# Kernel optimization log

Measured on AMD Instinct MI355X. Metric: run time of the kernel, lower is better.

Reference implementation:

```python
import jax, jax.numpy as jnp
import numpy as np

N = 20000      # nodes
E = 100000     # edges
B = 128        # graphs in batch
F_IN = 14      # node feature dim
DIM = 64       # hidden dim
E_FEAT = 4     # edge feature dim
MLP_H = 128    # edge MLP hidden


def setup_inputs() -> dict:
    key = jax.random.key(0)
    ks = jax.random.split(key, 26)

    def rn(k, shape, fan_in):
        return jax.random.normal(k, shape, jnp.float32) / np.sqrt(fan_in)

    d = {}
    d['x'] = jax.random.normal(ks[0], (N, F_IN), jnp.float32)
    d['edge_attr'] = jax.random.uniform(ks[1], (E, E_FEAT), jnp.float32)
    d['edge_index'] = jax.random.randint(ks[2], (2, E), 0, N)
    d['batch'] = jnp.sort(jax.random.randint(ks[3], (N,), 0, B))
    # lin0
    d['lin0_w'] = rn(ks[4], (F_IN, DIM), F_IN)
    d['lin0_b'] = jnp.zeros((DIM,), jnp.float32)
    # edge MLP: Linear(4,128) -> ReLU -> Linear(128, dim*dim)
    d['mlp_w1'] = rn(ks[5], (E_FEAT, MLP_H), E_FEAT)
    d['mlp_b1'] = jnp.zeros((MLP_H,), jnp.float32)
    d['mlp_w2'] = rn(ks[6], (MLP_H, DIM * DIM), MLP_H) * 0.1
    d['mlp_b2'] = jnp.zeros((DIM * DIM,), jnp.float32)
    # NNConv root weight + bias
    d['conv_root'] = rn(ks[7], (DIM, DIM), DIM)
    d['conv_bias'] = jnp.zeros((DIM,), jnp.float32)
    # GRU (input dim DIM, hidden DIM), torch gate order r,z,n
    d['gru_wi'] = rn(ks[8], (DIM, 3 * DIM), DIM)
    d['gru_wh'] = rn(ks[9], (DIM, 3 * DIM), DIM)
    d['gru_bi'] = jnp.zeros((3 * DIM,), jnp.float32)
    d['gru_bh'] = jnp.zeros((3 * DIM,), jnp.float32)
    # Set2Set LSTM (input 2*DIM, hidden DIM), torch gate order i,f,g,o
    d['lstm_wi'] = rn(ks[10], (2 * DIM, 4 * DIM), 2 * DIM)
    d['lstm_wh'] = rn(ks[11], (DIM, 4 * DIM), DIM)
    d['lstm_bi'] = jnp.zeros((4 * DIM,), jnp.float32)
    d['lstm_bh'] = jnp.zeros((4 * DIM,), jnp.float32)
    # output head
    d['lin1_w'] = rn(ks[12], (2 * DIM, DIM), 2 * DIM)
    d['lin1_b'] = jnp.zeros((DIM,), jnp.float32)
    d['lin2_w'] = rn(ks[13], (DIM, 1), DIM)
    d['lin2_b'] = jnp.zeros((1,), jnp.float32)
    return d


def _forward(x, edge_attr, edge_index, batch,
             lin0_w, lin0_b, mlp_w1, mlp_b1, mlp_w2, mlp_b2,
             conv_root, conv_bias,
             gru_wi, gru_wh, gru_bi, gru_bh,
             lstm_wi, lstm_wh, lstm_bi, lstm_bh,
             lin1_w, lin1_b, lin2_w, lin2_b):
    src, dst = edge_index[0], edge_index[1]

    out = jax.nn.relu(x @ lin0_w + lin0_b)            # [N, DIM]
    h = out                                            # GRU hidden

    # per-edge weight matrices from edge MLP (shared across the 3 steps)
    ew = jax.nn.relu(edge_attr @ mlp_w1 + mlp_b1) @ mlp_w2 + mlp_b2
    ew = ew.reshape(E, DIM, DIM)                       # [E, DIM, DIM]
    # incoming-edge counts for scatter-mean
    cnt = jax.ops.segment_sum(jnp.ones((E,), jnp.float32), dst, num_segments=N)
    cnt = jnp.maximum(cnt, 1.0)[:, None]

    for _ in range(3):
        msg = jnp.einsum('ei,eio->eo', out[src], ew)   # gather + per-edge matmul
        agg = jax.ops.segment_sum(msg, dst, num_segments=N) / cnt
        m = jax.nn.relu(agg + out @ conv_root + conv_bias)
        # GRU cell (torch gate order: r, z, n)
        gi = m @ gru_wi + gru_bi
        gh = h @ gru_wh + gru_bh
        r = jax.nn.sigmoid(gi[:, :DIM] + gh[:, :DIM])
        z = jax.nn.sigmoid(gi[:, DIM:2 * DIM] + gh[:, DIM:2 * DIM])
        n = jnp.tanh(gi[:, 2 * DIM:] + r * gh[:, 2 * DIM:])
        h = (1.0 - z) * n + z * h
        out = h

    # Set2Set pooling, 3 processing steps
    q_star = jnp.zeros((B, 2 * DIM), jnp.float32)
    hl = jnp.zeros((B, DIM), jnp.float32)
    cl = jnp.zeros((B, DIM), jnp.float32)
    for _ in range(3):
        gates = q_star @ lstm_wi + hl @ lstm_wh + lstm_bi + lstm_bh  # [B, 4*DIM]
        i = jax.nn.sigmoid(gates[:, :DIM])
        f = jax.nn.sigmoid(gates[:, DIM:2 * DIM])
        g = jnp.tanh(gates[:, 2 * DIM:3 * DIM])
        o = jax.nn.sigmoid(gates[:, 3 * DIM:])
        cl = f * cl + i * g
        hl = o * jnp.tanh(cl)
        q = hl                                         # [B, DIM]
        e = jnp.sum(out * q[batch], axis=-1)           # [N]
        emax = jax.ops.segment_max(e, batch, num_segments=B)
        emax = jnp.where(jnp.isfinite(emax), emax, 0.0)
        a = jnp.exp(e - emax[batch])
        asum = jax.ops.segment_sum(a, batch, num_segments=B)
        a = a / jnp.maximum(asum, 1e-16)[batch]
        r_vec = jax.ops.segment_sum(a[:, None] * out, batch, num_segments=B)
        q_star = jnp.concatenate([q, r_vec], axis=-1)  # [B, 2*DIM]

    y = jax.nn.relu(q_star @ lin1_w + lin1_b) @ lin2_w + lin2_b
    return y.reshape(-1)                               # [B]


def reference(x, edge_attr, edge_index, batch,
              lin0_w, lin0_b, mlp_w1, mlp_b1, mlp_w2, mlp_b2,
              conv_root, conv_bias,
              gru_wi, gru_wh, gru_bi, gru_bh,
              lstm_wi, lstm_wh, lstm_bi, lstm_bh,
              lin1_w, lin1_b, lin2_w, lin2_b):
    return _forward(x, edge_attr, edge_index, batch,
                    lin0_w, lin0_b, mlp_w1, mlp_b1, mlp_w2, mlp_b2,
                    conv_root, conv_bias,
                    gru_wi, gru_wh, gru_bi, gru_bh,
                    lstm_wi, lstm_wh, lstm_bi, lstm_bh,
                    lin1_w, lin1_b, lin2_w, lin2_b)
```

## Files before the change

kernel.cpp:

```cpp
#include <hip/hip_runtime.h>
#include <math.h>

#define N_ 20000
#define E_ 100000
#define B_ 128
#define F_IN_ 14
#define DIM_ 64
#define E_FEAT_ 4
#define MLP_H_ 128
#define EWC_ 4096
#define PC_ 8192
#define PC2_ 8256

typedef __attribute__((ext_vector_type(4))) float f32x4;
typedef __attribute__((ext_vector_type(8))) _Float16 halfx8;

__global__ void lin0_kernel(const float* __restrict__ x, const float* __restrict__ w,
                            const float* __restrict__ b, float* __restrict__ out) {
    int idx = blockIdx.x * blockDim.x + threadIdx.x;
    if (idx >= N_ * DIM_) return;
    int n = idx >> 6, d = idx & 63;
    float acc = b[d];
#pragma unroll
    for (int f = 0; f < F_IN_; ++f) acc = fmaf(x[n * F_IN_ + f], w[f * DIM_ + d], acc);
    out[idx] = acc > 0.f ? acc : 0.f;
}

__global__ void mlp1_kernel(const float* __restrict__ ea, const float* __restrict__ w1,
                            const float* __restrict__ b1, const int* __restrict__ epos,
                            _Float16* __restrict__ h1s) {
    int idx = blockIdx.x * blockDim.x + threadIdx.x;
    if (idx >= E_ * MLP_H_) return;
    int e = idx >> 7, k = idx & 127;
    float acc = b1[k];
#pragma unroll
    for (int f = 0; f < E_FEAT_; ++f) acc = fmaf(ea[e * E_FEAT_ + f], w1[f * MLP_H_ + k], acc);
    h1s[(size_t)epos[e] * 128 + k] = (_Float16)(acc > 0.f ? acc : 0.f);
}

__global__ void deg_kernel(const int* __restrict__ src, const int* __restrict__ dst,
                           float* __restrict__ cnt, int* __restrict__ cnt_src) {
    int e = blockIdx.x * blockDim.x + threadIdx.x;
    if (e >= E_) return;
    atomicAdd(&cnt[dst[e]], 1.0f);
    atomicAdd(&cnt_src[src[e]], 1);
}

__global__ void batch_off_kernel(const int* __restrict__ batch, int* __restrict__ off_b) {
    int b = threadIdx.x;
    if (b > B_) return;
    int lo = 0, hi = N_;
    while (lo < hi) {
        int mid = (lo + hi) >> 1;
        if (batch[mid] < b) lo = mid + 1; else hi = mid;
    }
    off_b[b] = lo;
}

__global__ void scan_src(const int* __restrict__ cnt_src, int* __restrict__ src_off) {
    __shared__ int part[256];
    __shared__ int off[257];
    int t = threadIdx.x;
    const int per = (N_ + 255) / 256;
    int base = t * per;
    int s = 0;
    for (int i = 0; i < per; ++i) { int b = base + i; if (b < N_) s += cnt_src[b]; }
    part[t] = s;
    __syncthreads();
    if (t == 0) {
        int a = 0;
        for (int i = 0; i < 256; ++i) { off[i] = a; a += part[i]; }
        off[256] = a;
    }
    __syncthreads();
    int run = off[t];
    for (int i = 0; i < per; ++i) {
        int b = base + i;
        if (b < N_) { src_off[b] = run; run += cnt_src[b]; }
    }
    if (t == 0) src_off[N_] = off[256];
}

__global__ void scatter_src(const int* __restrict__ src, const int* __restrict__ dst,
                            int* __restrict__ cur, const int* __restrict__ src_off,
                            int* __restrict__ epos, int* __restrict__ dsts) {
    int e = blockIdx.x * blockDim.x + threadIdx.x;
    if (e >= E_) return;
    int s = src[e];
    int p = src_off[s] + atomicAdd(&cur[s], 1);
    epos[e] = p;
    dsts[p] = dst[e];
}

__global__ void prep_b(const float* __restrict__ w2, const float* __restrict__ b2,
                       _Float16* __restrict__ Bf) {
    int idx = blockIdx.x * blockDim.x + threadIdx.x;
    if (idx >= PC2_ * 64) return;
    int c16 = idx >> 10;
    int r   = idx & 1023;
    int ks  = r >> 9;
    int q   = (r >> 7) & 3;
    int lr  = (r >> 3) & 15;
    int j   = r & 7;
    int c = c16 * 16 + lr;
    int i = ks * 32 + q * 8 + j;
    float v;
    if (c < PC_) {
        int o = c >> 7, k = c & 127;
        v = w2[(size_t)k * EWC_ + i * 64 + o];
    } else {
        int o = c - PC_;
        v = b2[i * 64 + o];
    }
    Bf[idx] = (_Float16)v;
}

__global__ __launch_bounds__(512, 4) void fused_msg(
        const float* __restrict__ out, const _Float16* __restrict__ Bf,
        const _Float16* __restrict__ h1s,
        const int* __restrict__ dsts, const int* __restrict__ src_off,
        float* __restrict__ agg) {
    __shared__ _Float16 Plds[16 * 2048];
    const int tid = threadIdx.x;
    const int lane = tid & 63;
    const int w = __builtin_amdgcn_readfirstlane(tid >> 6);
    const int lrow = lane & 15, quad = lane >> 4;
    const int nb0 = blockIdx.x * 16;

    halfx8 aG[2];
    {
        const float* orow = out + (size_t)(nb0 + lrow) * 64 + quad * 8;
#pragma unroll
        for (int ks = 0; ks < 2; ++ks) {
            float4 v0 = *(const float4*)(orow + ks * 32);
            float4 v1 = *(const float4*)(orow + ks * 32 + 4);
            aG[ks][0] = (_Float16)v0.x; aG[ks][1] = (_Float16)v0.y;
            aG[ks][2] = (_Float16)v0.z; aG[ks][3] = (_Float16)v0.w;
            aG[ks][4] = (_Float16)v1.x; aG[ks][5] = (_Float16)v1.y;
            aG[ks][6] = (_Float16)v1.z; aG[ks][7] = (_Float16)v1.w;
        }
    }

    f32x4 qf[4];
#pragma unroll
    for (int f = 0; f < 4; ++f) {
        const _Float16* bc = &Bf[(size_t)(512 + f) * 1024 + quad * 128 + lrow * 8];
        halfx8 bq0 = *(const halfx8*)bc;
        halfx8 bq1 = *(const halfx8*)(bc + 512);
        f32x4 z = (f32x4){0.f, 0.f, 0.f, 0.f};
        z = __builtin_amdgcn_mfma_f32_16x16x32_f16(aG[0], bq0, z, 0, 0, 0);
        z = __builtin_amdgcn_mfma_f32_16x16x32_f16(aG[1], bq1, z, 0, 0, 0);
        qf[f] = z;
    }

    const int n0g = nb0 + 2 * w;
    const int beg0 = src_off[n0g];
    const int end0 = src_off[n0g + 1];
    const int end1 = src_off[n0g + 2];

#pragma unroll
    for (int p = 0; p < 4; ++p) {
        if (p) __syncthreads();

#pragma unroll 8
        for (int nf = 0; nf < 16; ++nf) {
            int cl = w * 256 + nf * 16 + lrow;
            size_t tb = (size_t)(p * 128 + w * 16 + nf) * 1024 + quad * 128 + lrow * 8;
            halfx8 b0 = *(const halfx8*)&Bf[tb];
            halfx8 b1 = *(const halfx8*)&Bf[tb + 512];
            f32x4 acc = (f32x4){0.f, 0.f, 0.f, 0.f};
            acc = __builtin_amdgcn_mfma_f32_16x16x32_f16(aG[0], b0, acc, 0, 0, 0);
            acc = __builtin_amdgcn_mfma_f32_16x16x32_f16(aG[1], b1, acc, 0, 0, 0);
            int o = cl >> 7, k = cl & 127;
            int kz = k ^ (quad << 5) ^ ((o & 7) << 3);
            int base = o * 2048 + kz;
#pragma unroll
            for (int rr = 0; rr < 4; ++rr)
                Plds[base + (quad * 4 + rr) * 128] = (_Float16)acc[rr];
        }
        __syncthreads();

        int o0 = p * 16;
#pragma unroll
        for (int nn = 0; nn < 2; ++nn) {
            int nl = 2 * w + nn;
            int beg = nn ? end0 : beg0;
            int endv = nn ? end1 : end0;
            if (beg == endv) continue;
            int srcl = ((nl >> 2) << 4) | lrow;
            int rsel = nl & 3;
            float qel = rsel == 0 ? qf[p][0] : rsel == 1 ? qf[p][1]
                      : rsel == 2 ? qf[p][2] : qf[p][3];
            float qv = __shfl(qel, srcl, 64);
            halfx8 bf[4];
#pragma unroll
            for (int ks = 0; ks < 4; ++ks) {
                int kk = (ks * 32 + quad * 8) ^ ((nl >> 2) << 5) ^ ((lrow & 7) << 3);
                bf[ks] = *(const halfx8*)&Plds[lrow * 2048 + nl * 128 + kk];
            }
            for (int g = beg; g < endv; g += 16) {
                int gcnt = endv - g; if (gcnt > 16) gcnt = 16;
                int ei = lrow < gcnt ? lrow : gcnt - 1;
                int gi = g + ei;
                int dv = dsts[gi];
                halfx8 af[4];
#pragma unroll
                for (int ks = 0; ks < 4; ++ks)
                    af[ks] = *(const halfx8*)&h1s[(size_t)gi * 128 + ks * 32 + quad * 8];
                f32x4 acc = (f32x4){0.f, 0.f, 0.f, 0.f};
#pragma unroll
                for (int ks = 0; ks < 4; ++ks)
                    acc = __builtin_amdgcn_mfma_f32_16x16x32_f16(
                        af[ks], bf[ks], acc, 0, 0, 0);
#pragma unroll
                for (int rr = 0; rr < 4; ++rr) {
                    int j = quad * 4 + rr;
                    int d = __shfl(dv, j, 64);
                    if (j < gcnt) {
                        atomicAdd(&agg[(size_t)d * 64 + o0 + lrow], acc[rr] + qv);
                    }
                }
            }
        }
    }
}

__global__ __launch_bounds__(256) void gru_kernel(float* __restrict__ out,
                                                  float* __restrict__ agg,
                                                  const float* __restrict__ cnt,
                                                  const float* __restrict__ root,
                                                  const float* __restrict__ cbias,
                                                  const float* __restrict__ wi,
                                                  const float* __restrict__ wh,
                                                  const float* __restrict__ bi,
                                                  const float* __restrict__ bh) {
    __shared__ float root_s[64 * 64];
    __shared__ float h_s[32 * 64];
    __shared__ float m_s[32 * 64];
    int tid = threadIdx.x;
    int lane = tid & 63;
    int wv = __builtin_amdgcn_readfirstlane(tid >> 6);
    int nb = blockIdx.x * 32;
#pragma unroll
    for (int it = 0; it < 4; ++it) {
        int i = it * 1024 + tid * 4;
        *(float4*)&root_s[i] = *(const float4*)&root[i];
    }
#pragma unroll
    for (int it = 0; it < 2; ++it) {
        int i = it * 1024 + tid * 4;
        *(float4*)&h_s[i] = *(const float4*)&out[(size_t)nb * 64 + i];
    }
    __syncthreads();

    int nbase = nb + wv * 8;
    float a[8];
#pragma unroll
    for (int j = 0; j < 8; ++j) {
        int n = nbase + j;
        float c = cnt[n]; c = c > 1.f ? c : 1.f;
        a[j] = agg[(size_t)n * 64 + lane] / c + cbias[lane];
        agg[(size_t)n * 64 + lane] = 0.f;
    }
    for (int i = 0; i < 64; ++i) {
        float rv = root_s[i * 64 + lane];
#pragma unroll
        for (int j = 0; j < 8; ++j)
            a[j] = fmaf(h_s[(wv * 8 + j) * 64 + i], rv, a[j]);
    }
#pragma unroll
    for (int j = 0; j < 8; ++j) {
        float m = a[j] > 0.f ? a[j] : 0.f;
        m_s[(wv * 8 + j) * 64 + lane] = m;
    }
    __syncthreads();

    float gir[8], giz[8], gin[8], ghr[8], ghz[8], ghn[8];
    float bi0 = bi[lane], bi1 = bi[64 + lane], bi2 = bi[128 + lane];
    float bh0 = bh[lane], bh1 = bh[64 + lane], bh2 = bh[128 + lane];
#pragma unroll
    for (int j = 0; j < 8; ++j) {
        gir[j] = bi0; giz[j] = bi1; gin[j] = bi2;
        ghr[j] = bh0; ghz[j] = bh1; ghn[j] = bh2;
    }
    for (int i = 0; i < 64; ++i) {
        float w0 = wi[i * 192 + lane];
        float w1 = wi[i * 192 + 64 + lane];
        float w2v = wi[i * 192 + 128 + lane];
        float u0 = wh[i * 192 + lane];
        float u1 = wh[i * 192 + 64 + lane];
        float u2 = wh[i * 192 + 128 + lane];
#pragma unroll
        for (int j = 0; j < 8; ++j) {
            float mi = m_s[(wv * 8 + j) * 64 + i];
            float hi = h_s[(wv * 8 + j) * 64 + i];
            gir[j] = fmaf(mi, w0, gir[j]);
            giz[j] = fmaf(mi, w1, giz[j]);
            gin[j] = fmaf(mi, w2v, gin[j]);
            ghr[j] = fmaf(hi, u0, ghr[j]);
            ghz[j] = fmaf(hi, u1, ghz[j]);
            ghn[j] = fmaf(hi, u2, ghn[j]);
        }
    }
#pragma unroll
    for (int j = 0; j < 8; ++j) {
        int n = nbase + j;
        float rg = 1.f / (1.f + expf(-(gir[j] + ghr[j])));
        float zg = 1.f / (1.f + expf(-(giz[j] + ghz[j])));
        float ng = tanhf(gin[j] + rg * ghn[j]);
        float h = h_s[(wv * 8 + j) * 64 + lane];
        out[(size_t)n * 64 + lane] = (1.f - zg) * ng + zg * h;
    }
}

__global__ __launch_bounds__(256) void lstm_attn_kernel(
        const float* __restrict__ out, const int* __restrict__ off_b,
        float* __restrict__ hl, float* __restrict__ cl,
        float* __restrict__ q_star, float* __restrict__ e_ws,
        const float* __restrict__ wi, const float* __restrict__ wh,
        const float* __restrict__ bi, const float* __restrict__ bh,
        const float* __restrict__ hw1, const float* __restrict__ hb1,
        const float* __restrict__ hw2, const float* __restrict__ hb2,
        float* __restrict__ y, int do_head) {
    int b = blockIdx.x;
    int t = threadIdx.x;
    __shared__ float qs[128], hs[64], g[256];
    __shared__ float q[64];
    __shared__ float red[256], racc[256], sasum[4];

    if (t < 128) qs[t] = q_star[b * 128 + t];
    if (t < 64) hs[t] = hl[b * 64 + t];
    __syncthreads();
    {
        float acc = bi[t] + bh[t];
#pragma unroll 8
        for (int i = 0; i < 128; ++i) acc = fmaf(qs[i], wi[i * 256 + t], acc);
#pragma unroll 8
        for (int i = 0; i < 64; ++i) acc = fmaf(hs[i], wh[i * 256 + t], acc);
        g[t] = acc;
    }
    __syncthreads();
    if (t < 64) {
        float ig = 1.f / (1.f + expf(-g[t]));
        float fg = 1.f / (1.f + expf(-g[64 + t]));
        float gg = tanhf(g[128 + t]);
        float og = 1.f / (1.f + expf(-g[192 + t]));
        float c = fg * cl[b * 64 + t] + ig * gg;
        cl[b * 64 + t] = c;
        float h = og * tanhf(c);
        hl[b * 64 + t] = h;
        q[t] = h;
    }
    __syncthreads();

    int start = off_b[b], end = off_b[b + 1];
    float lmax = -1e30f;
    for (int n = start + t; n < end; n += 256) {
        float acc = 0.f;
#pragma unroll 16
        for (int d2 = 0; d2 < 64; ++d2) acc = fmaf(out[n * 64 + d2], q[d2], acc);
        e_ws[n] = acc;
        lmax = fmaxf(lmax, acc);
    }
    red[t] = lmax;
    __syncthreads();
    for (int s2 = 128; s2 > 0; s2 >>= 1) {
        if (t < s2) red[t] = fmaxf(red[t], red[t + s2]);
        __syncthreads();
    }
    float emax = red[0];
    int w = t >> 6, d = t & 63;
    float rl = 0.f, lasum = 0.f;
    for (int n = start + w; n < end; n += 4) {
        float a = expf(e_ws[n] - emax);
        rl = fmaf(a, out[n * 64 + d], rl);
        if (d == 0) lasum += a;
    }
    racc[t] = rl;
    if (d == 0) sasum[w] = lasum;
    __syncthreads();
    if (t < 64) {
        float r = racc[t] + racc[64 + t] + racc[128 + t] + racc[192 + t];
        float as = sasum[0] + sasum[1] + sasum[2] + sasum[3];
        as = fmaxf(as, 1e-16f);
        float rv = r / as;
        q_star[b * 128 + t] = q[t];
        q_star[b * 128 + 64 + t] = rv;
        qs[t] = q[t];
        qs[64 + t] = rv;
    }
    __syncthreads();

    if (do_head && t < 64) {
        float acc = hb1[t];
#pragma unroll 8
        for (int i = 0; i < 128; ++i) acc = fmaf(qs[i], hw1[i * 64 + t], acc);
        acc = acc > 0.f ? acc : 0.f;
        float p = acc * hw2[t];
        for (int off = 32; off > 0; off >>= 1) p += __shfl_down(p, off, 64);
        if (t == 0) y[b] = p + hb2[0];
    }
}

extern "C" void kernel_launch(void* const* d_in, const int* in_sizes, int n_in,
                              void* d_out, int out_size, void* d_ws, size_t ws_size,
                              hipStream_t stream) {
    (void)in_sizes; (void)n_in; (void)out_size; (void)ws_size;
    const float* x        = (const float*)d_in[0];
    const float* ea       = (const float*)d_in[1];
    const int*   eidx     = (const int*)d_in[2];
    const int*   batch    = (const int*)d_in[3];
    const float* lin0_w   = (const float*)d_in[4];
    const float* lin0_b   = (const float*)d_in[5];
    const float* mlp_w1   = (const float*)d_in[6];
    const float* mlp_b1   = (const float*)d_in[7];
    const float* mlp_w2   = (const float*)d_in[8];
    const float* mlp_b2   = (const float*)d_in[9];
    const float* conv_root= (const float*)d_in[10];
    const float* conv_bias= (const float*)d_in[11];
    const float* gru_wi   = (const float*)d_in[12];
    const float* gru_wh   = (const float*)d_in[13];
    const float* gru_bi   = (const float*)d_in[14];
    const float* gru_bh   = (const float*)d_in[15];
    const float* lstm_wi  = (const float*)d_in[16];
    const float* lstm_wh  = (const float*)d_in[17];
    const float* lstm_bi  = (const float*)d_in[18];
    const float* lstm_bh  = (const float*)d_in[19];
    const float* lin1_w   = (const float*)d_in[20];
    const float* lin1_b   = (const float*)d_in[21];
    const float* lin2_w   = (const float*)d_in[22];
    const float* lin2_b   = (const float*)d_in[23];
    float* y = (float*)d_out;

    const int* src = eidx;
    const int* dst = eidx + E_;

    char* w = (char*)d_ws;
    auto carve = [&](size_t bytes) {
        char* p = w;
        w += (bytes + 255) & ~(size_t)255;
        return p;
    };
    float* out_buf = (float*)carve((size_t)N_ * DIM_ * 4);
    float* e_ws    = (float*)carve((size_t)N_ * 4);
    int*   off_b   = (int*)carve((size_t)(B_ + 1) * 4);
    _Float16* h1s  = (_Float16*)carve((size_t)E_ * MLP_H_ * 2);
    _Float16* Bf   = (_Float16*)carve((size_t)PC2_ * 64 * 2);
    int*   src_off = (int*)carve((size_t)(N_ + 1) * 4);
    int*   epos    = (int*)carve((size_t)E_ * 4);
    int*   dsts    = (int*)carve((size_t)E_ * 4);
    char*  zero0   = w;
    float* agg     = (float*)carve((size_t)N_ * DIM_ * 4);
    float* cnt     = (float*)carve((size_t)N_ * 4);
    int*   cnt_src = (int*)carve((size_t)N_ * 4);
    int*   cur     = (int*)carve((size_t)N_ * 4);
    float* q_star  = (float*)carve((size_t)B_ * 128 * 4);
    float* hl      = (float*)carve((size_t)B_ * 64 * 4);
    float* cl      = (float*)carve((size_t)B_ * 64 * 4);
    size_t zbytes  = (size_t)(w - zero0);

    hipMemsetAsync(zero0, 0, zbytes, stream);

    lin0_kernel<<<(N_ * DIM_ + 255) / 256, 256, 0, stream>>>(x, lin0_w, lin0_b, out_buf);
    deg_kernel<<<(E_ + 255) / 256, 256, 0, stream>>>(src, dst, cnt, cnt_src);
    batch_off_kernel<<<1, 256, 0, stream>>>(batch, off_b);
    scan_src<<<1, 256, 0, stream>>>(cnt_src, src_off);
    scatter_src<<<(E_ + 255) / 256, 256, 0, stream>>>(src, dst, cur, src_off, epos, dsts);
    mlp1_kernel<<<(E_ * MLP_H_ + 255) / 256, 256, 0, stream>>>(ea, mlp_w1, mlp_b1, epos, h1s);
    prep_b<<<(PC2_ * 64 + 255) / 256, 256, 0, stream>>>(mlp_w2, mlp_b2, Bf);

    for (int step = 0; step < 3; ++step) {
        fused_msg<<<N_ / 16, 512, 0, stream>>>(out_buf, Bf, h1s, dsts,
                                               src_off, agg);
        gru_kernel<<<N_ / 32, 256, 0, stream>>>(out_buf, agg, cnt, conv_root, conv_bias,
                                                gru_wi, gru_wh, gru_bi, gru_bh);
    }

    for (int s = 0; s < 3; ++s) {
        lstm_attn_kernel<<<B_, 256, 0, stream>>>(out_buf, off_b, hl, cl, q_star, e_ws,
                                                 lstm_wi, lstm_wh, lstm_bi, lstm_bh,
                                                 lin1_w, lin1_b, lin2_w, lin2_b,
                                                 y, s == 2 ? 1 : 0);
    }
}
```

Measured before the change: 603.9 us.

## Process 32 source nodes per block to reuse weight tiles across two node groups

```diff
diff --git a/kernel.cpp b/kernel.cpp
--- a/kernel.cpp
+++ b/kernel.cpp
@@ -120,83 +120,105 @@
         const _Float16* __restrict__ h1s,
         const int* __restrict__ dsts, const int* __restrict__ src_off,
         float* __restrict__ agg) {
-    __shared__ _Float16 Plds[16 * 2048];
+    __shared__ _Float16 Plds[8 * 4096];
     const int tid = threadIdx.x;
     const int lane = tid & 63;
     const int w = __builtin_amdgcn_readfirstlane(tid >> 6);
     const int lrow = lane & 15, quad = lane >> 4;
-    const int nb0 = blockIdx.x * 16;
-
-    halfx8 aG[2];
+    const int lr7 = lrow & 7;
+    const int nb0 = blockIdx.x * 32;
+
+    halfx8 aA[2], aB[2];
     {
-        const float* orow = out + (size_t)(nb0 + lrow) * 64 + quad * 8;
+        const float* orowA = out + (size_t)(nb0 + lrow) * 64 + quad * 8;
+        const float* orowB = out + (size_t)(nb0 + 16 + lrow) * 64 + quad * 8;
 #pragma unroll
         for (int ks = 0; ks < 2; ++ks) {
-            float4 v0 = *(const float4*)(orow + ks * 32);
-            float4 v1 = *(const float4*)(orow + ks * 32 + 4);
-            aG[ks][0] = (_Float16)v0.x; aG[ks][1] = (_Float16)v0.y;
-            aG[ks][2] = (_Float16)v0.z; aG[ks][3] = (_Float16)v0.w;
-            aG[ks][4] = (_Float16)v1.x; aG[ks][5] = (_Float16)v1.y;
-            aG[ks][6] = (_Float16)v1.z; aG[ks][7] = (_Float16)v1.w;
+            float4 v0 = *(const float4*)(orowA + ks * 32);
+            float4 v1 = *(const float4*)(orowA + ks * 32 + 4);
+            aA[ks][0] = (_Float16)v0.x; aA[ks][1] = (_Float16)v0.y;
+            aA[ks][2] = (_Float16)v0.z; aA[ks][3] = (_Float16)v0.w;
+            aA[ks][4] = (_Float16)v1.x; aA[ks][5] = (_Float16)v1.y;
+            aA[ks][6] = (_Float16)v1.z; aA[ks][7] = (_Float16)v1.w;
+            float4 u0 = *(const float4*)(orowB + ks * 32);
+            float4 u1 = *(const float4*)(orowB + ks * 32 + 4);
+            aB[ks][0] = (_Float16)u0.x; aB[ks][1] = (_Float16)u0.y;
+            aB[ks][2] = (_Float16)u0.z; aB[ks][3] = (_Float16)u0.w;
+            aB[ks][4] = (_Float16)u1.x; aB[ks][5] = (_Float16)u1.y;
+            aB[ks][6] = (_Float16)u1.z; aB[ks][7] = (_Float16)u1.w;
         }
     }
 
-    f32x4 qf[4];
+    f32x4 qfA[4], qfB[4];
 #pragma unroll
     for (int f = 0; f < 4; ++f) {
         const _Float16* bc = &Bf[(size_t)(512 + f) * 1024 + quad * 128 + lrow * 8];
         halfx8 bq0 = *(const halfx8*)bc;
         halfx8 bq1 = *(const halfx8*)(bc + 512);
         f32x4 z = (f32x4){0.f, 0.f, 0.f, 0.f};
-        z = __builtin_amdgcn_mfma_f32_16x16x32_f16(aG[0], bq0, z, 0, 0, 0);
-        z = __builtin_amdgcn_mfma_f32_16x16x32_f16(aG[1], bq1, z, 0, 0, 0);
-        qf[f] = z;
-    }
-
-    const int n0g = nb0 + 2 * w;
-    const int beg0 = src_off[n0g];
-    const int end0 = src_off[n0g + 1];
-    const int end1 = src_off[n0g + 2];
-
-#pragma unroll
-    for (int p = 0; p < 4; ++p) {
+        z = __builtin_amdgcn_mfma_f32_16x16x32_f16(aA[0], bq0, z, 0, 0, 0);
+        z = __builtin_amdgcn_mfma_f32_16x16x32_f16(aA[1], bq1, z, 0, 0, 0);
+        qfA[f] = z;
+        f32x4 z2 = (f32x4){0.f, 0.f, 0.f, 0.f};
+        z2 = __builtin_amdgcn_mfma_f32_16x16x32_f16(aB[0], bq0, z2, 0, 0, 0);
+        z2 = __builtin_amdgcn_mfma_f32_16x16x32_f16(aB[1], bq1, z2, 0, 0, 0);
+        qfB[f] = z2;
+    }
+
+    const int nA = nb0 + 2 * w;
+    const int nB = nb0 + 16 + 2 * w;
+    const int begA0 = src_off[nA], endA0 = src_off[nA + 1], endA1 = src_off[nA + 2];
+    const int begB0 = src_off[nB], endB0 = src_off[nB + 1], endB1 = src_off[nB + 2];
+
+#pragma unroll
+    for (int p = 0; p < 8; ++p) {
         if (p) __syncthreads();
 
-#pragma unroll 8
-        for (int nf = 0; nf < 16; ++nf) {
-            int cl = w * 256 + nf * 16 + lrow;
-            size_t tb = (size_t)(p * 128 + w * 16 + nf) * 1024 + quad * 128 + lrow * 8;
+#pragma unroll
+        for (int it = 0; it < 8; ++it) {
+            int f64 = w * 8 + it;
+            size_t tb = (size_t)(p * 64 + f64) * 1024 + quad * 128 + lrow * 8;
             halfx8 b0 = *(const halfx8*)&Bf[tb];
             halfx8 b1 = *(const halfx8*)&Bf[tb + 512];
-            f32x4 acc = (f32x4){0.f, 0.f, 0.f, 0.f};
-            acc = __builtin_amdgcn_mfma_f32_16x16x32_f16(aG[0], b0, acc, 0, 0, 0);
-            acc = __builtin_amdgcn_mfma_f32_16x16x32_f16(aG[1], b1, acc, 0, 0, 0);
+            f32x4 accA = (f32x4){0.f, 0.f, 0.f, 0.f};
+            f32x4 accB = (f32x4){0.f, 0.f, 0.f, 0.f};
+            accA = __builtin_amdgcn_mfma_f32_16x16x32_f16(aA[0], b0, accA, 0, 0, 0);
+            accA = __builtin_amdgcn_mfma_f32_16x16x32_f16(aA[1], b1, accA, 0, 0, 0);
+            accB = __builtin_amdgcn_mfma_f32_16x16x32_f16(aB[0], b0, accB, 0, 0, 0);
+            accB = __builtin_amdgcn_mfma_f32_16x16x32_f16(aB[1], b1, accB, 0, 0, 0);
+            int cl = f64 * 16 + lrow;
             int o = cl >> 7, k = cl & 127;
-            int kz = k ^ (quad << 5) ^ ((o & 7) << 3);
-            int base = o * 2048 + kz;
-#pragma unroll
-            for (int rr = 0; rr < 4; ++rr)
-                Plds[base + (quad * 4 + rr) * 128] = (_Float16)acc[rr];
+            int kz = k ^ (quad << 5) ^ (o << 3);
+            int base = o * 4096 + kz;
+#pragma unroll
+            for (int rr = 0; rr < 4; ++rr) {
+                Plds[base + (quad * 4 + rr) * 128] = (_Float16)accA[rr];
+                Plds[base + (16 + quad * 4 + rr) * 128] = (_Float16)accB[rr];
+            }
         }
         __syncthreads();
 
-        int o0 = p * 16;
-#pragma unroll
-        for (int nn = 0; nn < 2; ++nn) {
-            int nl = 2 * w + nn;
-            int beg = nn ? end0 : beg0;
-            int endv = nn ? end1 : end0;
+        int o0 = p * 8;
+#pragma unroll
+        for (int nn = 0; nn < 4; ++nn) {
+            int nl15 = 2 * w + (nn & 1);
+            int nl = ((nn >> 1) << 4) | nl15;
+            int beg  = (nn == 0) ? begA0 : (nn == 1) ? endA0
+                     : (nn == 2) ? begB0 : endB0;
+            int endv = (nn == 0) ? endA0 : (nn == 1) ? endA1
+                     : (nn == 2) ? endB0 : endB1;
             if (beg == endv) continue;
-            int srcl = ((nl >> 2) << 4) | lrow;
-            int rsel = nl & 3;
-            float qel = rsel == 0 ? qf[p][0] : rsel == 1 ? qf[p][1]
-                      : rsel == 2 ? qf[p][2] : qf[p][3];
+            f32x4 qq = (nn >> 1) ? qfB[p >> 1] : qfA[p >> 1];
+            int rsel = nl15 & 3;
+            float qel = rsel == 0 ? qq[0] : rsel == 1 ? qq[1]
+                      : rsel == 2 ? qq[2] : qq[3];
+            int srcl = ((nl15 >> 2) << 4) | (((p & 1) << 3) | lr7);
             float qv = __shfl(qel, srcl, 64);
             halfx8 bf[4];
 #pragma unroll
             for (int ks = 0; ks < 4; ++ks) {
-                int kk = (ks * 32 + quad * 8) ^ ((nl >> 2) << 5) ^ ((lrow & 7) << 3);
-                bf[ks] = *(const halfx8*)&Plds[lrow * 2048 + nl * 128 + kk];
+                int kk = (ks * 32 + quad * 8) ^ (((nl >> 2) & 3) << 5) ^ (lr7 << 3);
+                bf[ks] = *(const halfx8*)&Plds[lr7 * 4096 + nl * 128 + kk];
             }
             for (int g = beg; g < endv; g += 16) {
                 int gcnt = endv - g; if (gcnt > 16) gcnt = 16;
@@ -216,8 +238,8 @@
                 for (int rr = 0; rr < 4; ++rr) {
                     int j = quad * 4 + rr;
                     int d = __shfl(dv, j, 64);
-                    if (j < gcnt) {
-                        atomicAdd(&agg[(size_t)d * 64 + o0 + lrow], acc[rr] + qv);
+                    if (j < gcnt && lrow < 8) {
+                        atomicAdd(&agg[(size_t)d * 64 + o0 + lr7], acc[rr] + qv);
                     }
                 }
             }
@@ -470,7 +492,7 @@
     prep_b<<<(PC2_ * 64 + 255) / 256, 256, 0, stream>>>(mlp_w2, mlp_b2, Bf);
 
     for (int step = 0; step < 3; ++step) {
-        fused_msg<<<N_ / 16, 512, 0, stream>>>(out_buf, Bf, h1s, dsts,
+        fused_msg<<<N_ / 32, 512, 0, stream>>>(out_buf, Bf, h1s, dsts,
                                                src_off, agg);
         gru_kernel<<<N_ / 32, 256, 0, stream>>>(out_buf, agg, cnt, conv_root, conv_bias,
                                                 gru_wi, gru_wh, gru_bi, gru_bh);
```

New measurement: 696.4 us. +15.3%, slower.

## Fuse setup kernels and merge three Set2Set LSTM steps into one launch

Applied to the files above, without the earlier changes.

```diff
diff --git a/kernel.cpp b/kernel.cpp
--- a/kernel.cpp
+++ b/kernel.cpp
@@ -26,35 +26,23 @@
     out[idx] = acc > 0.f ? acc : 0.f;
 }
 
-__global__ void mlp1_kernel(const float* __restrict__ ea, const float* __restrict__ w1,
-                            const float* __restrict__ b1, const int* __restrict__ epos,
-                            _Float16* __restrict__ h1s) {
-    int idx = blockIdx.x * blockDim.x + threadIdx.x;
-    if (idx >= E_ * MLP_H_) return;
-    int e = idx >> 7, k = idx & 127;
-    float acc = b1[k];
-#pragma unroll
-    for (int f = 0; f < E_FEAT_; ++f) acc = fmaf(ea[e * E_FEAT_ + f], w1[f * MLP_H_ + k], acc);
-    h1s[(size_t)epos[e] * 128 + k] = (_Float16)(acc > 0.f ? acc : 0.f);
-}
-
-__global__ void deg_kernel(const int* __restrict__ src, const int* __restrict__ dst,
-                           float* __restrict__ cnt, int* __restrict__ cnt_src) {
+__global__ void deg_boff_kernel(const int* __restrict__ src, const int* __restrict__ dst,
+                                float* __restrict__ cnt, int* __restrict__ cnt_src,
+                                const int* __restrict__ batch, int* __restrict__ off_b) {
     int e = blockIdx.x * blockDim.x + threadIdx.x;
-    if (e >= E_) return;
-    atomicAdd(&cnt[dst[e]], 1.0f);
-    atomicAdd(&cnt_src[src[e]], 1);
-}
-
-__global__ void batch_off_kernel(const int* __restrict__ batch, int* __restrict__ off_b) {
-    int b = threadIdx.x;
-    if (b > B_) return;
-    int lo = 0, hi = N_;
-    while (lo < hi) {
-        int mid = (lo + hi) >> 1;
-        if (batch[mid] < b) lo = mid + 1; else hi = mid;
-    }
-    off_b[b] = lo;
+    if (e < E_) {
+        atomicAdd(&cnt[dst[e]], 1.0f);
+        atomicAdd(&cnt_src[src[e]], 1);
+    }
+    if (blockIdx.x == 0 && threadIdx.x <= B_) {
+        int b = threadIdx.x;
+        int lo = 0, hi = N_;
+        while (lo < hi) {
+            int mid = (lo + hi) >> 1;
+            if (batch[mid] < b) lo = mid + 1; else hi = mid;
+        }
+        off_b[b] = lo;
+    }
 }
 
 __global__ void scan_src(const int* __restrict__ cnt_src, int* __restrict__ src_off) {
@@ -81,15 +69,41 @@
     if (t == 0) src_off[N_] = off[256];
 }
 
-__global__ void scatter_src(const int* __restrict__ src, const int* __restrict__ dst,
-                            int* __restrict__ cur, const int* __restrict__ src_off,
-                            int* __restrict__ epos, int* __restrict__ dsts) {
-    int e = blockIdx.x * blockDim.x + threadIdx.x;
+__global__ __launch_bounds__(256) void scatter_mlp1(
+        const int* __restrict__ src, const int* __restrict__ dst,
+        int* __restrict__ cur, const int* __restrict__ src_off,
+        const float* __restrict__ ea, const float* __restrict__ w1,
+        const float* __restrict__ b1, int* __restrict__ dsts,
+        _Float16* __restrict__ h1s) {
+    __shared__ float w1s[E_FEAT_ * MLP_H_];
+    __shared__ float b1s[MLP_H_];
+    int t = threadIdx.x;
+    if (t < MLP_H_) b1s[t] = b1[t];
+    for (int i = t; i < E_FEAT_ * MLP_H_; i += 256) w1s[i] = w1[i];
+    __syncthreads();
+    int e = blockIdx.x * 256 + t;
     if (e >= E_) return;
     int s = src[e];
     int p = src_off[s] + atomicAdd(&cur[s], 1);
-    epos[e] = p;
     dsts[p] = dst[e];
+    float a0 = ea[e * 4 + 0], a1 = ea[e * 4 + 1];
+    float a2 = ea[e * 4 + 2], a3 = ea[e * 4 + 3];
+    _Float16* hrow = h1s + (size_t)p * 128;
+#pragma unroll
+    for (int k8 = 0; k8 < 16; ++k8) {
+        halfx8 v;
+#pragma unroll
+        for (int j = 0; j < 8; ++j) {
+            int k = k8 * 8 + j;
+            float acc = b1s[k];
+            acc = fmaf(a0, w1s[k], acc);
+            acc = fmaf(a1, w1s[128 + k], acc);
+            acc = fmaf(a2, w1s[256 + k], acc);
+            acc = fmaf(a3, w1s[384 + k], acc);
+            v[j] = (_Float16)(acc > 0.f ? acc : 0.f);
+        }
+        *(halfx8*)&hrow[k8 * 8] = v;
+    }
 }
 
 __global__ void prep_b(const float* __restrict__ w2, const float* __restrict__ b2,
@@ -313,85 +327,85 @@
     }
 }
 
-__global__ __launch_bounds__(256) void lstm_attn_kernel(
+__global__ __launch_bounds__(256) void lstm_all_kernel(
         const float* __restrict__ out, const int* __restrict__ off_b,
-        float* __restrict__ hl, float* __restrict__ cl,
-        float* __restrict__ q_star, float* __restrict__ e_ws,
+        float* __restrict__ e_ws,
         const float* __restrict__ wi, const float* __restrict__ wh,
         const float* __restrict__ bi, const float* __restrict__ bh,
         const float* __restrict__ hw1, const float* __restrict__ hb1,
         const float* __restrict__ hw2, const float* __restrict__ hb2,
-        float* __restrict__ y, int do_head) {
+        float* __restrict__ y) {
     int b = blockIdx.x;
     int t = threadIdx.x;
-    __shared__ float qs[128], hs[64], g[256];
+    __shared__ float qs[128], hs[64], cs[64], g[256];
     __shared__ float q[64];
     __shared__ float red[256], racc[256], sasum[4];
 
-    if (t < 128) qs[t] = q_star[b * 128 + t];
-    if (t < 64) hs[t] = hl[b * 64 + t];
-    __syncthreads();
-    {
-        float acc = bi[t] + bh[t];
+    if (t < 128) qs[t] = 0.f;
+    if (t < 64) { hs[t] = 0.f; cs[t] = 0.f; }
+    __syncthreads();
+
+    int start = off_b[b], end = off_b[b + 1];
+
+    for (int s = 0; s < 3; ++s) {
+        {
+            float acc = bi[t] + bh[t];
 #pragma unroll 8
-        for (int i = 0; i < 128; ++i) acc = fmaf(qs[i], wi[i * 256 + t], acc);
+            for (int i = 0; i < 128; ++i) acc = fmaf(qs[i], wi[i * 256 + t], acc);
 #pragma unroll 8
-        for (int i = 0; i < 64; ++i) acc = fmaf(hs[i], wh[i * 256 + t], acc);
-        g[t] = acc;
-    }
-    __syncthreads();
+            for (int i = 0; i < 64; ++i) acc = fmaf(hs[i], wh[i * 256 + t], acc);
+            g[t] = acc;
+        }
+        __syncthreads();
+        if (t < 64) {
+            float ig = 1.f / (1.f + expf(-g[t]));
+            float fg = 1.f / (1.f + expf(-g[64 + t]));
+            float gg = tanhf(g[128 + t]);
+            float og = 1.f / (1.f + expf(-g[192 + t]));
+            float c = fg * cs[t] + ig * gg;
+            cs[t] = c;
+            float h = og * tanhf(c);
+            hs[t] = h;
+            q[t] = h;
+        }
+        __syncthreads();
+
+        float lmax = -1e30f;
+        for (int n = start + t; n < end; n += 256) {
+            float acc = 0.f;
+#pragma unroll 16
+            for (int d2 = 0; d2 < 64; ++d2) acc = fmaf(out[n * 64 + d2], q[d2], acc);
+            e_ws[n] = acc;
+            lmax = fmaxf(lmax, acc);
+        }
+        red[t] = lmax;
+        __syncthreads();
+        for (int s2 = 128; s2 > 0; s2 >>= 1) {
+            if (t < s2) red[t] = fmaxf(red[t], red[t + s2]);
+            __syncthreads();
+        }
+        float emax = red[0];
+        int w = t >> 6, d = t & 63;
+        float rl = 0.f, lasum = 0.f;
+        for (int n = start + w; n < end; n += 4) {
+            float a = expf(e_ws[n] - emax);
+            rl = fmaf(a, out[n * 64 + d], rl);
+            if (d == 0) lasum += a;
+        }
+        racc[t] = rl;
+        if (d == 0) sasum[w] = lasum;
+        __syncthreads();
+        if (t < 64) {
+            float r = racc[t] + racc[64 + t] + racc[128 + t] + racc[192 + t];
+            float as = sasum[0] + sasum[1] + sasum[2] + sasum[3];
+            as = fmaxf(as, 1e-16f);
+            qs[t] = q[t];
+            qs[64 + t] = r / as;
+        }
+        __syncthreads();
+    }
+
     if (t < 64) {
-        float ig = 1.f / (1.f + expf(-g[t]));
-        float fg = 1.f / (1.f + expf(-g[64 + t]));
-        float gg = tanhf(g[128 + t]);
-        float og = 1.f / (1.f + expf(-g[192 + t]));
-        float c = fg * cl[b * 64 + t] + ig * gg;
-        cl[b * 64 + t] = c;
-        float h = og * tanhf(c);
-        hl[b * 64 + t] = h;
-        q[t] = h;
-    }
-    __syncthreads();
-
-    int start = off_b[b], end = off_b[b + 1];
-    float lmax = -1e30f;
-    for (int n = start + t; n < end; n += 256) {
-        float acc = 0.f;
-#pragma unroll 16
-        for (int d2 = 0; d2 < 64; ++d2) acc = fmaf(out[n * 64 + d2], q[d2], acc);
-        e_ws[n] = acc;
-        lmax = fmaxf(lmax, acc);
-    }
-    red[t] = lmax;
-    __syncthreads();
-    for (int s2 = 128; s2 > 0; s2 >>= 1) {
-        if (t < s2) red[t] = fmaxf(red[t], red[t + s2]);
-        __syncthreads();
-    }
-    float emax = red[0];
-    int w = t >> 6, d = t & 63;
-    float rl = 0.f, lasum = 0.f;
-    for (int n = start + w; n < end; n += 4) {
-        float a = expf(e_ws[n] - emax);
-        rl = fmaf(a, out[n * 64 + d], rl);
-        if (d == 0) lasum += a;
-    }
-    racc[t] = rl;
-    if (d == 0) sasum[w] = lasum;
-    __syncthreads();
-    if (t < 64) {
-        float r = racc[t] + racc[64 + t] + racc[128 + t] + racc[192 + t];
-        float as = sasum[0] + sasum[1] + sasum[2] + sasum[3];
-        as = fmaxf(as, 1e-16f);
-        float rv = r / as;
-        q_star[b * 128 + t] = q[t];
-        q_star[b * 128 + 64 + t] = rv;
-        qs[t] = q[t];
-        qs[64 + t] = rv;
-    }
-    __syncthreads();
-
-    if (do_head && t < 64) {
         float acc = hb1[t];
 #pragma unroll 8
         for (int i = 0; i < 128; ++i) acc = fmaf(qs[i], hw1[i * 64 + t], acc);
@@ -447,26 +461,23 @@
     _Float16* h1s  = (_Float16*)carve((size_t)E_ * MLP_H_ * 2);
     _Float16* Bf   = (_Float16*)carve((size_t)PC2_ * 64 * 2);
     int*   src_off = (int*)carve((size_t)(N_ + 1) * 4);
-    int*   epos    = (int*)carve((size_t)E_ * 4);
     int*   dsts    = (int*)carve((size_t)E_ * 4);
     char*  zero0   = w;
     float* agg     = (float*)carve((size_t)N_ * DIM_ * 4);
     float* cnt     = (float*)carve((size_t)N_ * 4);
     int*   cnt_src = (int*)carve((size_t)N_ * 4);
     int*   cur     = (int*)carve((size_t)N_ * 4);
-    float* q_star  = (float*)carve((size_t)B_ * 128 * 4);
-    float* hl      = (float*)carve((size_t)B_ * 64 * 4);
-    float* cl      = (float*)carve((size_t)B_ * 64 * 4);
     size_t zbytes  = (size_t)(w - zero0);
 
     hipMemsetAsync(zero0, 0, zbytes, stream);
 
     lin0_kernel<<<(N_ * DIM_ + 255) / 256, 256, 0, stream>>>(x, lin0_w, lin0_b, out_buf);
-    deg_kernel<<<(E_ + 255) / 256, 256, 0, stream>>>(src, dst, cnt, cnt_src);
-    batch_off_kernel<<<1, 256, 0, stream>>>(batch, off_b);
+    deg_boff_kernel<<<(E_ + 255) / 256, 256, 0, stream>>>(src, dst, cnt, cnt_src,
+                                                          batch, off_b);
     scan_src<<<1, 256, 0, stream>>>(cnt_src, src_off);
-    scatter_src<<<(E_ + 255) / 256, 256, 0, stream>>>(src, dst, cur, src_off, epos, dsts);
-    mlp1_kernel<<<(E_ * MLP_H_ + 255) / 256, 256, 0, stream>>>(ea, mlp_w1, mlp_b1, epos, h1s);
+    scatter_mlp1<<<(E_ + 255) / 256, 256, 0, stream>>>(src, dst, cur, src_off,
+                                                       ea, mlp_w1, mlp_b1,
+                                                       dsts, h1s);
     prep_b<<<(PC2_ * 64 + 255) / 256, 256, 0, stream>>>(mlp_w2, mlp_b2, Bf);
 
     for (int step = 0; step < 3; ++step) {
@@ -476,10 +487,7 @@
                                                 gru_wi, gru_wh, gru_bi, gru_bh);
     }
 
-    for (int s = 0; s < 3; ++s) {
-        lstm_attn_kernel<<<B_, 256, 0, stream>>>(out_buf, off_b, hl, cl, q_star, e_ws,
-                                                 lstm_wi, lstm_wh, lstm_bi, lstm_bh,
-                                                 lin1_w, lin1_b, lin2_w, lin2_b,
-                                                 y, s == 2 ? 1 : 0);
-    }
-}
+    lstm_all_kernel<<<B_, 256, 0, stream>>>(out_buf, off_b, e_ws,
+                                            lstm_wi, lstm_wh, lstm_bi, lstm_bh,
+                                            lin1_w, lin1_b, lin2_w, lin2_b, y);
+}
```

Result: faster. 582.8 us (-3.5%).
